# Kernel tuning notes

Measured on AMD Instinct MI355X. Metric: run time of the kernel, lower is better.

The kernel has to match this reference:

```python
import jax, jax.numpy as jnp
import numpy as np

N = 50000
E = 800000
D_IN, D_HID, D_OUT = 128, 128, 64
BN_EPS = 1e-5

def _glorot(key, shape):
    fan_in = shape[-1]
    return jax.random.normal(key, shape, dtype=jnp.float32) / jnp.sqrt(jnp.float32(fan_in))

def setup_inputs() -> dict:
    key = jax.random.key(0)
    ks = jax.random.split(key, 16)
    x = jax.random.normal(ks[0], (N, D_IN), dtype=jnp.float32)
    edge_index = jax.random.randint(ks[1], (2, E), 0, N, dtype=jnp.int64)
    edge_pairs = jax.random.randint(ks[2], (2, E), 0, N, dtype=jnp.int64)
    return {
        "x": x,
        "edge_index": edge_index,
        "edge_pairs": edge_pairs,
        # SAGEConv1: lin_l (bias) on aggregated neighbors, lin_r (no bias) on root
        "c1_Wl": _glorot(ks[3], (D_HID, D_IN)),
        "c1_bl": jnp.zeros((D_HID,), jnp.float32),
        "c1_Wr": _glorot(ks[4], (D_HID, D_IN)),
        # BatchNorm1d (eval mode: running stats)
        "bn_gamma": jnp.ones((D_HID,), jnp.float32),
        "bn_beta": jnp.zeros((D_HID,), jnp.float32),
        "bn_mean": jnp.zeros((D_HID,), jnp.float32),
        "bn_var": jnp.ones((D_HID,), jnp.float32),
        # SAGEConv2
        "c2_Wl": _glorot(ks[5], (D_OUT, D_HID)),
        "c2_bl": jnp.zeros((D_OUT,), jnp.float32),
        "c2_Wr": _glorot(ks[6], (D_OUT, D_HID)),
        # EdgeRegHead MLP: Linear(2*D_OUT, D_OUT) -> ReLU -> Linear(D_OUT, D_OUT//2) -> ReLU -> Linear(D_OUT//2, 1) -> Sigmoid
        "e_W1": _glorot(ks[7], (D_OUT, 2 * D_OUT)),
        "e_b1": jnp.zeros((D_OUT,), jnp.float32),
        "e_W2": _glorot(ks[8], (D_OUT // 2, D_OUT)),
        "e_b2": jnp.zeros((D_OUT // 2,), jnp.float32),
        "e_W3": _glorot(ks[9], (1, D_OUT // 2)),
        "e_b3": jnp.zeros((1,), jnp.float32),
    }

def _sage_conv(x, src, dst, Wl, bl, Wr):
    # mean-aggregate source features at destination nodes (PyG SAGEConv mean aggr)
    msg_sum = jax.ops.segment_sum(x[src], dst, num_segments=N)          # [N, d]
    cnt = jax.ops.segment_sum(jnp.ones((src.shape[0],), x.dtype), dst, num_segments=N)
    mean = msg_sum / jnp.maximum(cnt, 1.0)[:, None]
    return mean @ Wl.T + bl + x @ Wr.T

def reference(x, edge_index, edge_pairs,
              c1_Wl, c1_bl, c1_Wr,
              bn_gamma, bn_beta, bn_mean, bn_var,
              c2_Wl, c2_bl, c2_Wr,
              e_W1, e_b1, e_W2, e_b2, e_W3, e_b3):
    src, dst = edge_index[0], edge_index[1]
    h = _sage_conv(x, src, dst, c1_Wl, c1_bl, c1_Wr)                    # [N, D_HID]
    h = (h - bn_mean) * jax.lax.rsqrt(bn_var + BN_EPS) * bn_gamma + bn_beta
    h = jax.nn.relu(h)                                                   # dropout inactive (eval)
    z = _sage_conv(h, src, dst, c2_Wl, c2_bl, c2_Wr)                    # [N, D_OUT]
    zi = z[edge_pairs[0]]                                               # [P, D_OUT]
    zj = z[edge_pairs[1]]
    e = jnp.concatenate([zi, zj], axis=-1)                              # [P, 2*D_OUT]
    e = jax.nn.relu(e @ e_W1.T + e_b1)
    e = jax.nn.relu(e @ e_W2.T + e_b2)
    return jax.nn.sigmoid(e @ e_W3.T + e_b3)                            # [P, 1]
```

## Files before the change

### kernel.cpp

```cpp
#include <hip/hip_runtime.h>
#include <hip/hip_bf16.h>
#include <math.h>

#define NN 50000
#define NE 800000
#define DIN 128
#define DHID 128
#define DOUT 64
#define BN_EPS 1e-5f

typedef __attribute__((ext_vector_type(8))) short bf16x8;
typedef __attribute__((ext_vector_type(8))) _Float16 f16x8;
typedef __attribute__((ext_vector_type(4))) _Float16 f16x4;
typedef __attribute__((ext_vector_type(2))) _Float16 f16x2;
typedef __attribute__((ext_vector_type(4))) float f32x4;
typedef unsigned short ushort_t;
typedef unsigned int uint_t;

__device__ __forceinline__ ushort_t f2bf(float f) {
    uint_t u = __float_as_uint(f);
    uint_t r = (u + 0x7FFFu + ((u >> 16) & 1u)) >> 16;
    return (ushort_t)r;
}

__device__ __forceinline__ uint_t pk2bf(float a, float b) {
    __hip_bfloat16 x = __float2bfloat16(a);
    __hip_bfloat16 y = __float2bfloat16(b);
    ushort_t ux = *reinterpret_cast<ushort_t*>(&x);
    ushort_t uy = *reinterpret_cast<ushort_t*>(&y);
    return (uint_t)ux | ((uint_t)uy << 16);
}

__global__ __launch_bounds__(256) void k_deg_xcast(
    const int* __restrict__ ei, int* __restrict__ deg,
    const float* __restrict__ x, _Float16* __restrict__ xh)
{
    int b = blockIdx.x;
    if (b < 3125) {
        int e = b * 256 + threadIdx.x;
        atomicAdd(deg + ei[NE + e], 1);
    } else {
        int i = (b - 3125) * 256 + threadIdx.x;
        const float4* src = (const float4*)x + (size_t)i * 2;
        float4 a = src[0], c = src[1];
        f16x8 o;
        o[0] = (_Float16)a.x; o[1] = (_Float16)a.y; o[2] = (_Float16)a.z; o[3] = (_Float16)a.w;
        o[4] = (_Float16)c.x; o[5] = (_Float16)c.y; o[6] = (_Float16)c.z; o[7] = (_Float16)c.w;
        *(f16x8*)(xh + (size_t)i * 8) = o;
    }
}

__global__ __launch_bounds__(256) void k_scan1_prep(
    const int* __restrict__ deg, int* __restrict__ part,
    const float* __restrict__ c1_Wl, const float* __restrict__ c1_Wr,
    const float* __restrict__ c2_Wl, const float* __restrict__ c2_Wr,
    const float* __restrict__ gam, const float* __restrict__ bet,
    const float* __restrict__ bmean, const float* __restrict__ bvar,
    const float* __restrict__ eW1, const float* __restrict__ eW2,
    _Float16* __restrict__ w1cat, _Float16* __restrict__ w2cat,
    ushort_t* __restrict__ w1bf, ushort_t* __restrict__ w2bf,
    float* __restrict__ bnsc, float* __restrict__ bnsh)
{
    int t = threadIdx.x;
    if (blockIdx.x < 49) {
        __shared__ int s[256];
        int g = blockIdx.x * 256 + t;
        int v = 0;
        if (g < 12500) { int4 d = ((const int4*)deg)[g]; v = d.x + d.y + d.z + d.w; }
        s[t] = v;
        __syncthreads();
        #pragma unroll
        for (int off = 128; off > 0; off >>= 1) {
            if (t < off) s[t] += s[t + off];
            __syncthreads();
        }
        if (t == 0) part[blockIdx.x] = s[0];
    } else {
        for (int i = t; i < 128 * 128; i += 256) {
            int row = i >> 7, k = i & 127;
            w1cat[row * 256 + k]       = (_Float16)c1_Wl[i];
            w1cat[row * 256 + 128 + k] = (_Float16)c1_Wr[i];
        }
        for (int i = t; i < 64 * 128; i += 256) {
            int row = i >> 7, k = i & 127;
            w2cat[row * 256 + k]       = (_Float16)c2_Wl[i];
            w2cat[row * 256 + 128 + k] = (_Float16)c2_Wr[i];
        }
        for (int i = t; i < 64 * 128; i += 256) w1bf[i] = f2bf(eW1[i]);
        for (int i = t; i < 32 * 64; i += 256)  w2bf[i] = f2bf(eW2[i]);
        for (int i = t; i < 128; i += 256) {
            float s = gam[i] * rsqrtf(bvar[i] + BN_EPS);
            bnsc[i] = s;
            bnsh[i] = bet[i] - bmean[i] * s;
        }
    }
}

__global__ __launch_bounds__(256) void k_scan3(
    const int* __restrict__ deg, const int* __restrict__ part, int* __restrict__ rowptr)
{
    __shared__ int s[256];
    __shared__ int p[64];
    int t = threadIdx.x;
    int b = blockIdx.x;
    int g = b * 256 + t;
    int4 d = make_int4(0, 0, 0, 0);
    if (g < 12500) d = ((const int4*)deg)[g];
    int sum4 = d.x + d.y + d.z + d.w;
    s[t] = sum4;
    if (t < 49) p[t] = part[t];
    __syncthreads();
    #pragma unroll
    for (int off = 1; off < 256; off <<= 1) {
        int v = (t >= off) ? s[t - off] : 0;
        __syncthreads();
        s[t] += v;
        __syncthreads();
    }
    int blockoff = 0;
    for (int i = 0; i < b; ++i) blockoff += p[i];
    int off0 = blockoff + s[t] - sum4;
    if (g < 12500) {
        int4 o;
        o.x = off0;
        o.y = off0 + d.x;
        o.z = o.y + d.y;
        o.w = o.z + d.z;
        ((int4*)rowptr)[g] = o;
        if (g == 12499) rowptr[NN] = o.w + d.w;
    }
}

__global__ __launch_bounds__(256) void k_fill(
    const int* __restrict__ ei, const int* __restrict__ rowptr,
    int* __restrict__ cursor, int* __restrict__ csr_src)
{
    int e = blockIdx.x * blockDim.x + threadIdx.x;
    if (e >= NE) return;
    int dst = ei[NE + e];
    int slot = atomicAdd(cursor + dst, 1);
    csr_src[rowptr[dst] + slot] = ei[e];
}

#define GATHER4_128(feat)                                                      \
    {                                                                          \
        _Pragma("unroll 1")                                                    \
        for (int q = 0; q < 4; ++q) {                                          \
            int n = w * 4 + q;                                                 \
            int node4 = tile * 16 + n;                                         \
            int beg = __builtin_amdgcn_readfirstlane(rowptr[node4]);           \
            int end = __builtin_amdgcn_readfirstlane(rowptr[node4 + 1]);       \
            float2 a0 = {0.f,0.f}, a1 = {0.f,0.f}, a2 = {0.f,0.f}, a3 = {0.f,0.f}; \
            float2 a4 = {0.f,0.f}, a5 = {0.f,0.f}, a6 = {0.f,0.f}, a7 = {0.f,0.f}; \
            int j = beg;                                                       \
            for (; j + 7 < end; j += 8) {                                      \
                int s0 = csr_src[j];     int s1 = csr_src[j + 1];              \
                int s2 = csr_src[j + 2]; int s3 = csr_src[j + 3];              \
                int s4 = csr_src[j + 4]; int s5 = csr_src[j + 5];              \
                int s6 = csr_src[j + 6]; int s7 = csr_src[j + 7];              \
                f16x2 v0 = *(const f16x2*)(feat + (size_t)s0 * 128 + lane * 2);\
                f16x2 v1 = *(const f16x2*)(feat + (size_t)s1 * 128 + lane * 2);\
                f16x2 v2 = *(const f16x2*)(feat + (size_t)s2 * 128 + lane * 2);\
                f16x2 v3 = *(const f16x2*)(feat + (size_t)s3 * 128 + lane * 2);\
                f16x2 v4 = *(const f16x2*)(feat + (size_t)s4 * 128 + lane * 2);\
                f16x2 v5 = *(const f16x2*)(feat + (size_t)s5 * 128 + lane * 2);\
                f16x2 v6 = *(const f16x2*)(feat + (size_t)s6 * 128 + lane * 2);\
                f16x2 v7 = *(const f16x2*)(feat + (size_t)s7 * 128 + lane * 2);\
                a0.x += (float)v0[0]; a0.y += (float)v0[1];                    \
                a1.x += (float)v1[0]; a1.y += (float)v1[1];                    \
                a2.x += (float)v2[0]; a2.y += (float)v2[1];                    \
                a3.x += (float)v3[0]; a3.y += (float)v3[1];                    \
                a4.x += (float)v4[0]; a4.y += (float)v4[1];                    \
                a5.x += (float)v5[0]; a5.y += (float)v5[1];                    \
                a6.x += (float)v6[0]; a6.y += (float)v6[1];                    \
                a7.x += (float)v7[0]; a7.y += (float)v7[1];                    \
            }                                                                  \
            for (; j + 1 < end; j += 2) {                                      \
                int s0 = csr_src[j];                                           \
                int s1 = csr_src[j + 1];                                       \
                f16x2 v0 = *(const f16x2*)(feat + (size_t)s0 * 128 + lane * 2);\
                f16x2 v1 = *(const f16x2*)(feat + (size_t)s1 * 128 + lane * 2);\
                a0.x += (float)v0[0]; a0.y += (float)v0[1];                    \
                a1.x += (float)v1[0]; a1.y += (float)v1[1];                    \
            }                                                                  \
            if (j < end) {                                                     \
                int s0 = csr_src[j];                                           \
                f16x2 v0 = *(const f16x2*)(feat + (size_t)s0 * 128 + lane * 2);\
                a0.x += (float)v0[0]; a0.y += (float)v0[1];                    \
            }                                                                  \
            float inv = 1.0f / fmaxf((float)(end - beg), 1.0f);                \
            f16x2 o;                                                           \
            o[0] = (_Float16)((a0.x + a1.x + a2.x + a3.x + a4.x + a5.x + a6.x + a7.x) * inv); \
            o[1] = (_Float16)((a0.y + a1.y + a2.y + a3.y + a4.y + a5.y + a6.y + a7.y) * inv); \
            uint_t off = (uint_t)(n * 256 + lane * 4) ^ (uint_t)((n & 7) << 4);\
            *(f16x2*)((char*)mlds + off) = o;                                  \
        }                                                                      \
    }

__global__ __launch_bounds__(256) void k_gconv1(
    const _Float16* __restrict__ xh, const int* __restrict__ rowptr,
    const int* __restrict__ csr_src,
    const _Float16* __restrict__ w1cat, const float* __restrict__ bl,
    const float* __restrict__ bnsc, const float* __restrict__ bnsh,
    _Float16* __restrict__ hh)
{
    __shared__ _Float16 mlds[16 * 128];
    const int tid = threadIdx.x;
    const int lane = tid & 63;
    const int w = tid >> 6;
    const int tile = blockIdx.x;
    const int e = lane & 15;
    const int c = lane >> 4;
    const int node = tile * 16 + e;

    f16x8 wf[2][8];
    #pragma unroll
    for (int nt = 0; nt < 2; ++nt)
        #pragma unroll
        for (int ks = 0; ks < 8; ++ks)
            wf[nt][ks] = *(const f16x8*)(w1cat + (size_t)(w * 32 + nt * 16 + e) * 256 + ks * 32 + c * 8);
    f16x8 bfx[4];
    #pragma unroll
    for (int ks = 0; ks < 4; ++ks)
        bfx[ks] = *(const f16x8*)(xh + (size_t)node * 128 + ks * 32 + c * 8);
    f32x4 acc[2];
    #pragma unroll
    for (int nt = 0; nt < 2; ++nt)
        acc[nt] = *(const f32x4*)(bl + w * 32 + nt * 16 + c * 4);

    GATHER4_128(xh);
    __syncthreads();

    f16x8 bfm[4];
    #pragma unroll
    for (int ks = 0; ks < 4; ++ks) {
        uint_t off = (uint_t)(e * 256 + ks * 64 + c * 16) ^ (uint_t)((e & 7) << 4);
        bfm[ks] = *(const f16x8*)((const char*)mlds + off);
    }

    #pragma unroll
    for (int ks = 0; ks < 4; ++ks)
        #pragma unroll
        for (int nt = 0; nt < 2; ++nt)
            acc[nt] = __builtin_amdgcn_mfma_f32_16x16x32_f16(wf[nt][ks], bfm[ks], acc[nt], 0, 0, 0);
    #pragma unroll
    for (int ks = 0; ks < 4; ++ks)
        #pragma unroll
        for (int nt = 0; nt < 2; ++nt)
            acc[nt] = __builtin_amdgcn_mfma_f32_16x16x32_f16(wf[nt][ks + 4], bfx[ks], acc[nt], 0, 0, 0);

    #pragma unroll
    for (int nt = 0; nt < 2; ++nt) {
        int j0 = w * 32 + nt * 16 + c * 4;
        f32x4 sc = *(const f32x4*)(bnsc + j0);
        f32x4 sh = *(const f32x4*)(bnsh + j0);
        f16x4 o;
        #pragma unroll
        for (int r = 0; r < 4; ++r)
            o[r] = (_Float16)fmaxf(acc[nt][r] * sc[r] + sh[r], 0.f);
        *(f16x4*)(hh + (size_t)node * 128 + j0) = o;
    }
}

__global__ __launch_bounds__(256) void k_hw(
    const _Float16* __restrict__ hh, const _Float16* __restrict__ w2cat,
    _Float16* __restrict__ hw)
{
    const int tid = threadIdx.x;
    const int lane = tid & 63;
    const int e = lane & 15;
    const int c = lane >> 4;
    const int w = tid >> 6;
    const int node = blockIdx.x * 16 + e;

    f16x8 wf[4];
    #pragma unroll
    for (int ks = 0; ks < 4; ++ks)
        wf[ks] = *(const f16x8*)(w2cat + (size_t)(w * 16 + e) * 256 + ks * 32 + c * 8);
    f16x8 bf[4];
    #pragma unroll
    for (int ks = 0; ks < 4; ++ks)
        bf[ks] = *(const f16x8*)(hh + (size_t)node * 128 + ks * 32 + c * 8);

    f32x4 acc = {0.f, 0.f, 0.f, 0.f};
    #pragma unroll
    for (int ks = 0; ks < 4; ++ks)
        acc = __builtin_amdgcn_mfma_f32_16x16x32_f16(wf[ks], bf[ks], acc, 0, 0, 0);

    f16x4 o;
    #pragma unroll
    for (int r = 0; r < 4; ++r) o[r] = (_Float16)acc[r];
    *(f16x4*)(hw + (size_t)node * 64 + w * 16 + c * 4) = o;
}

__global__ __launch_bounds__(256) void k_gconv2(
    const _Float16* __restrict__ hh, const _Float16* __restrict__ hw,
    const int* __restrict__ rowptr, const int* __restrict__ csr_src,
    const _Float16* __restrict__ w2cat, const float* __restrict__ bl,
    ushort_t* __restrict__ zbf)
{
    __shared__ float mlds32[16 * 64];
    const int tid = threadIdx.x;
    const int lane = tid & 63;
    const int w = tid >> 6;
    const int tile = blockIdx.x;
    const int e = lane & 15;
    const int c = lane >> 4;
    const int node = tile * 16 + e;

    f16x8 wf[4];
    #pragma unroll
    for (int ks = 0; ks < 4; ++ks)
        wf[ks] = *(const f16x8*)(w2cat + (size_t)(w * 16 + e) * 256 + 128 + ks * 32 + c * 8);
    f16x8 bfx[4];
    #pragma unroll
    for (int ks = 0; ks < 4; ++ks)
        bfx[ks] = *(const f16x8*)(hh + (size_t)node * 128 + ks * 32 + c * 8);

    #pragma unroll 1
    for (int q = 0; q < 4; ++q) {
        int n = w * 4 + q;
        int node4 = tile * 16 + n;
        int beg = __builtin_amdgcn_readfirstlane(rowptr[node4]);
        int end = __builtin_amdgcn_readfirstlane(rowptr[node4 + 1]);
        float a0 = 0.f, a1 = 0.f, a2 = 0.f, a3 = 0.f;
        float a4 = 0.f, a5 = 0.f, a6 = 0.f, a7 = 0.f;
        int j = beg;
        for (; j + 7 < end; j += 8) {
            int s0 = csr_src[j];     int s1 = csr_src[j + 1];
            int s2 = csr_src[j + 2]; int s3 = csr_src[j + 3];
            int s4 = csr_src[j + 4]; int s5 = csr_src[j + 5];
            int s6 = csr_src[j + 6]; int s7 = csr_src[j + 7];
            a0 += (float)hw[(size_t)s0 * 64 + lane];
            a1 += (float)hw[(size_t)s1 * 64 + lane];
            a2 += (float)hw[(size_t)s2 * 64 + lane];
            a3 += (float)hw[(size_t)s3 * 64 + lane];
            a4 += (float)hw[(size_t)s4 * 64 + lane];
            a5 += (float)hw[(size_t)s5 * 64 + lane];
            a6 += (float)hw[(size_t)s6 * 64 + lane];
            a7 += (float)hw[(size_t)s7 * 64 + lane];
        }
        for (; j + 1 < end; j += 2) {
            int s0 = csr_src[j];
            int s1 = csr_src[j + 1];
            a0 += (float)hw[(size_t)s0 * 64 + lane];
            a1 += (float)hw[(size_t)s1 * 64 + lane];
        }
        if (j < end) {
            int s0 = csr_src[j];
            a0 += (float)hw[(size_t)s0 * 64 + lane];
        }
        float inv = 1.0f / fmaxf((float)(end - beg), 1.0f);
        float m = (a0 + a1 + a2 + a3 + a4 + a5 + a6 + a7) * inv;
        uint_t off = (uint_t)(n * 256 + lane * 4) ^ (uint_t)((n & 7) << 4);
        *(float*)((char*)mlds32 + off) = m;
    }
    __syncthreads();

    f32x4 acc = *(const f32x4*)(bl + w * 16 + c * 4);
    {
        uint_t off = (uint_t)(e * 256 + (w * 16 + c * 4) * 4) ^ (uint_t)((e & 7) << 4);
        f32x4 mv = *(const f32x4*)((const char*)mlds32 + off);
        acc[0] += mv[0]; acc[1] += mv[1]; acc[2] += mv[2]; acc[3] += mv[3];
    }

    #pragma unroll
    for (int ks = 0; ks < 4; ++ks)
        acc = __builtin_amdgcn_mfma_f32_16x16x32_f16(wf[ks], bfx[ks], acc, 0, 0, 0);

    int j0 = w * 16 + c * 4;
    uint2 pk;
    pk.x = pk2bf(acc[0], acc[1]);
    pk.y = pk2bf(acc[2], acc[3]);
    *(uint2*)(zbf + (size_t)node * 64 + j0) = pk;
}

__global__ __launch_bounds__(256) void k_edge(
    const ushort_t* __restrict__ zbf, const int* __restrict__ ep,
    const ushort_t* __restrict__ w1bf, const float* __restrict__ b1,
    const ushort_t* __restrict__ w2bf, const float* __restrict__ b2,
    const float* __restrict__ W3, const float* __restrict__ b3,
    float* __restrict__ out)
{
    __shared__ ushort_t a1lds[4][16 * 64];
    const int tid  = threadIdx.x;
    const int lane = tid & 63;
    const int e    = lane & 15;
    const int c    = lane >> 4;
    ushort_t* lds  = &a1lds[tid >> 6][0];
    const uint_t swz = (uint_t)((e & 7) << 4);

    bf16x8 w1f[4][4];
    #pragma unroll
    for (int mt = 0; mt < 4; ++mt)
        #pragma unroll
        for (int ks = 0; ks < 4; ++ks)
            w1f[mt][ks] = *(const bf16x8*)(w1bf + (mt * 16 + e) * 128 + ks * 32 + c * 8);

    bf16x8 w2f[2][2];
    #pragma unroll
    for (int mt2 = 0; mt2 < 2; ++mt2)
        #pragma unroll
        for (int ks2 = 0; ks2 < 2; ++ks2)
            w2f[mt2][ks2] = *(const bf16x8*)(w2bf + (mt2 * 16 + e) * 64 + ks2 * 32 + c * 8);

    f32x4 bias1[4];
    #pragma unroll
    for (int mt = 0; mt < 4; ++mt) bias1[mt] = *(const f32x4*)(b1 + mt * 16 + c * 4);
    f32x4 bias2[2];
    #pragma unroll
    for (int mt2 = 0; mt2 < 2; ++mt2) bias2[mt2] = *(const f32x4*)(b2 + mt2 * 16 + c * 4);
    f32x4 w3v[2];
    #pragma unroll
    for (int mt2 = 0; mt2 < 2; ++mt2) w3v[mt2] = *(const f32x4*)(W3 + mt2 * 16 + c * 4);
    const float b3v = b3[0];

    const int nw = (gridDim.x * blockDim.x) >> 6;
    const int NT = NE / 16;

#define LOADZ(T, dst)                                                         \
    {                                                                         \
        int p = (T) * 16 + e;                                                 \
        int ni = ep[p];                                                       \
        int nj = ep[NE + p];                                                  \
        const ushort_t* zi = zbf + (size_t)ni * DOUT;                         \
        const ushort_t* zj = zbf + (size_t)nj * DOUT;                         \
        dst[0] = *(const bf16x8*)(zi + c * 8);                                \
        dst[1] = *(const bf16x8*)(zi + 32 + c * 8);                           \
        dst[2] = *(const bf16x8*)(zj + c * 8);                                \
        dst[3] = *(const bf16x8*)(zj + 32 + c * 8);                           \
    }

#define COMPUTE(T, bfr)                                                       \
    {                                                                         \
        f32x4 acc[4];                                                         \
        _Pragma("unroll")                                                     \
        for (int mt = 0; mt < 4; ++mt) acc[mt] = bias1[mt];                   \
        _Pragma("unroll")                                                     \
        for (int ks = 0; ks < 4; ++ks)                                        \
            _Pragma("unroll")                                                 \
            for (int mt = 0; mt < 4; ++mt)                                    \
                acc[mt] = __builtin_amdgcn_mfma_f32_16x16x32_bf16(            \
                    w1f[mt][ks], bfr[ks], acc[mt], 0, 0, 0);                  \
        _Pragma("unroll")                                                     \
        for (int mt = 0; mt < 4; ++mt) {                                      \
            uint_t lo = pk2bf(fmaxf(acc[mt][0], 0.f), fmaxf(acc[mt][1], 0.f));\
            uint_t hi = pk2bf(fmaxf(acc[mt][2], 0.f), fmaxf(acc[mt][3], 0.f));\
            uint_t off = (uint_t)(e * 128 + mt * 32 + c * 8) ^ swz;           \
            *(uint2*)((char*)lds + off) = make_uint2(lo, hi);                 \
        }                                                                     \
        bf16x8 b2f[2];                                                        \
        _Pragma("unroll")                                                     \
        for (int ks2 = 0; ks2 < 2; ++ks2) {                                   \
            uint_t off = (uint_t)(e * 128 + ks2 * 64 + c * 16) ^ swz;         \
            b2f[ks2] = *(const bf16x8*)((const char*)lds + off);              \
        }                                                                     \
        f32x4 a2[2];                                                          \
        _Pragma("unroll")                                                     \
        for (int mt2 = 0; mt2 < 2; ++mt2) a2[mt2] = bias2[mt2];               \
        _Pragma("unroll")                                                     \
        for (int ks2 = 0; ks2 < 2; ++ks2)                                     \
            _Pragma("unroll")                                                 \
            for (int mt2 = 0; mt2 < 2; ++mt2)                                 \
                a2[mt2] = __builtin_amdgcn_mfma_f32_16x16x32_bf16(            \
                    w2f[mt2][ks2], b2f[ks2], a2[mt2], 0, 0, 0);               \
        float t3 = b3v;                                                       \
        _Pragma("unroll")                                                     \
        for (int mt2 = 0; mt2 < 2; ++mt2)                                     \
            _Pragma("unroll")                                                 \
            for (int r = 0; r < 4; ++r)                                       \
                t3 += fmaxf(a2[mt2][r], 0.f) * w3v[mt2][r];                   \
        t3 += __shfl_xor(t3, 16);                                             \
        t3 += __shfl_xor(t3, 32);                                             \
        if (lane < 16) {                                                      \
            float ex = __expf(-t3);                                           \
            out[(T) * 16 + lane] = __builtin_amdgcn_rcpf(1.f + ex);           \
        }                                                                     \
    }

    bf16x8 zA[4], zB[4];
    int tile = (blockIdx.x * blockDim.x + tid) >> 6;
    if (tile >= NT) return;
    LOADZ(tile, zA);
    while (tile < NT) {
        int nx = tile + nw;
        if (nx < NT) LOADZ(nx, zB);
        COMPUTE(tile, zA);
        tile = nx;
        if (tile >= NT) break;
        nx = tile + nw;
        if (nx < NT) LOADZ(nx, zA);
        COMPUTE(tile, zB);
        tile = nx;
    }

#undef LOADZ
#undef COMPUTE
}

extern "C" void kernel_launch(void* const* d_in, const int* in_sizes, int n_in,
                              void* d_out, int out_size, void* d_ws, size_t ws_size,
                              hipStream_t stream)
{
    const float* x     = (const float*)d_in[0];
    const int*   ei    = (const int*)d_in[1];
    const int*   ep    = (const int*)d_in[2];
    const float* c1_Wl = (const float*)d_in[3];
    const float* c1_bl = (const float*)d_in[4];
    const float* c1_Wr = (const float*)d_in[5];
    const float* bn_g  = (const float*)d_in[6];
    const float* bn_b  = (const float*)d_in[7];
    const float* bn_m  = (const float*)d_in[8];
    const float* bn_v  = (const float*)d_in[9];
    const float* c2_Wl = (const float*)d_in[10];
    const float* c2_bl = (const float*)d_in[11];
    const float* c2_Wr = (const float*)d_in[12];
    const float* e_W1  = (const float*)d_in[13];
    const float* e_b1  = (const float*)d_in[14];
    const float* e_W2  = (const float*)d_in[15];
    const float* e_b2  = (const float*)d_in[16];
    const float* e_W3  = (const float*)d_in[17];
    const float* e_b3  = (const float*)d_in[18];
    float* out = (float*)d_out;

    _Float16* xh    = (_Float16*)d_ws;
    _Float16* hwbuf = xh + (size_t)NN * DIN;
    _Float16* hh    = hwbuf + (size_t)NN * DIN;
    ushort_t* zbf   = (ushort_t*)(hh + (size_t)NN * DHID);
    _Float16* w1cat = (_Float16*)(zbf + (size_t)NN * DOUT);
    _Float16* w2cat = w1cat + 128 * 256;
    ushort_t* w1bf  = (ushort_t*)(w2cat + 64 * 256);
    ushort_t* w2bf  = w1bf + 64 * 128;
    float*    bnsc  = (float*)(w2bf + 32 * 64);
    float*    bnsh  = bnsc + 128;
    int*      deg     = (int*)(bnsh + 128);
    int*      cursor  = deg + 50048;
    int*      rowptr  = cursor + 50048;
    int*      csr_src = rowptr + 50052;
    int*      part    = csr_src + 800000;

    hipMemsetAsync(deg, 0, (size_t)(50048 * 2) * sizeof(int), stream);

    k_deg_xcast<<<6250, 256, 0, stream>>>(ei, deg, x, xh);
    k_scan1_prep<<<50, 256, 0, stream>>>(deg, part,
                                         c1_Wl, c1_Wr, c2_Wl, c2_Wr,
                                         bn_g, bn_b, bn_m, bn_v, e_W1, e_W2,
                                         w1cat, w2cat, w1bf, w2bf, bnsc, bnsh);
    k_scan3<<<49, 256, 0, stream>>>(deg, part, rowptr);
    k_fill <<<3125, 256, 0, stream>>>(ei, rowptr, cursor, csr_src);

    k_gconv1<<<3125, 256, 0, stream>>>(xh, rowptr, csr_src, w1cat, c1_bl, bnsc, bnsh, hh);
    k_hw    <<<3125, 256, 0, stream>>>(hh, w2cat, hwbuf);
    k_gconv2<<<3125, 256, 0, stream>>>(hh, hwbuf, rowptr, csr_src, w2cat, c2_bl, zbf);

    k_edge<<<1024, 256, 0, stream>>>(zbf, ep, w1bf, e_b1, w2bf, e_b2,
                                     e_W3, e_b3, out);
}
```

Baseline: 284.0 us.

## Fuse hidden-to-output projection into gconv1 and triple-buffer edge head loads

The separate k_hw kernel is folded into k_gconv1. Each block now writes its 16x128 post-BN/ReLU hidden tile into a swizzled LDS buffer and immediately multiplies it by the second-layer weights, so the hidden tile is not re-read from global memory and one launch goes away. The edge MLP kernel moves from double- to triple-buffered z-row gathers so more loads are in flight while computing. The trade-off is extra LDS, a block barrier and more registers in gconv1, plus more registers in k_edge, which may reduce occupancy.

```diff
diff --git a/kernel.cpp b/kernel.cpp
--- a/kernel.cpp
+++ b/kernel.cpp
@@ -202,9 +202,11 @@
     const int* __restrict__ csr_src,
     const _Float16* __restrict__ w1cat, const float* __restrict__ bl,
     const float* __restrict__ bnsc, const float* __restrict__ bnsh,
-    _Float16* __restrict__ hh)
+    const _Float16* __restrict__ w2cat, _Float16* __restrict__ hh,
+    _Float16* __restrict__ hw)
 {
     __shared__ _Float16 mlds[16 * 128];
+    __shared__ _Float16 hlds[16 * 128];
     const int tid = threadIdx.x;
     const int lane = tid & 63;
     const int w = tid >> 6;
@@ -259,38 +261,31 @@
         for (int r = 0; r < 4; ++r)
             o[r] = (_Float16)fmaxf(acc[nt][r] * sc[r] + sh[r], 0.f);
         *(f16x4*)(hh + (size_t)node * 128 + j0) = o;
-    }
-}
-
-__global__ __launch_bounds__(256) void k_hw(
-    const _Float16* __restrict__ hh, const _Float16* __restrict__ w2cat,
-    _Float16* __restrict__ hw)
-{
-    const int tid = threadIdx.x;
-    const int lane = tid & 63;
-    const int e = lane & 15;
-    const int c = lane >> 4;
-    const int w = tid >> 6;
-    const int node = blockIdx.x * 16 + e;
-
-    f16x8 wf[4];
-    #pragma unroll
-    for (int ks = 0; ks < 4; ++ks)
-        wf[ks] = *(const f16x8*)(w2cat + (size_t)(w * 16 + e) * 256 + ks * 32 + c * 8);
-    f16x8 bf[4];
-    #pragma unroll
-    for (int ks = 0; ks < 4; ++ks)
-        bf[ks] = *(const f16x8*)(hh + (size_t)node * 128 + ks * 32 + c * 8);
-
-    f32x4 acc = {0.f, 0.f, 0.f, 0.f};
-    #pragma unroll
-    for (int ks = 0; ks < 4; ++ks)
-        acc = __builtin_amdgcn_mfma_f32_16x16x32_f16(wf[ks], bf[ks], acc, 0, 0, 0);
-
-    f16x4 o;
-    #pragma unroll
-    for (int r = 0; r < 4; ++r) o[r] = (_Float16)acc[r];
-    *(f16x4*)(hw + (size_t)node * 64 + w * 16 + c * 4) = o;
+        uint_t hoff = (uint_t)(e * 256 + j0 * 2) ^ (uint_t)((e & 7) << 4);
+        *(f16x4*)((char*)hlds + hoff) = o;
+    }
+
+    f16x8 wf2[4];
+    #pragma unroll
+    for (int ks = 0; ks < 4; ++ks)
+        wf2[ks] = *(const f16x8*)(w2cat + (size_t)(w * 16 + e) * 256 + ks * 32 + c * 8);
+    __syncthreads();
+
+    f16x8 bfh[4];
+    #pragma unroll
+    for (int ks = 0; ks < 4; ++ks) {
+        uint_t off = (uint_t)(e * 256 + ks * 64 + c * 16) ^ (uint_t)((e & 7) << 4);
+        bfh[ks] = *(const f16x8*)((const char*)hlds + off);
+    }
+    f32x4 acc2 = {0.f, 0.f, 0.f, 0.f};
+    #pragma unroll
+    for (int ks = 0; ks < 4; ++ks)
+        acc2 = __builtin_amdgcn_mfma_f32_16x16x32_f16(wf2[ks], bfh[ks], acc2, 0, 0, 0);
+
+    f16x4 ohw;
+    #pragma unroll
+    for (int r = 0; r < 4; ++r) ohw[r] = (_Float16)acc2[r];
+    *(f16x4*)(hw + (size_t)node * 64 + w * 16 + c * 4) = ohw;
 }
 
 __global__ __launch_bounds__(256) void k_gconv2(
@@ -478,20 +473,27 @@
         }                                                                     \
     }
 
-    bf16x8 zA[4], zB[4];
-    int tile = (blockIdx.x * blockDim.x + tid) >> 6;
-    if (tile >= NT) return;
-    LOADZ(tile, zA);
-    while (tile < NT) {
-        int nx = tile + nw;
-        if (nx < NT) LOADZ(nx, zB);
-        COMPUTE(tile, zA);
-        tile = nx;
-        if (tile >= NT) break;
-        nx = tile + nw;
-        if (nx < NT) LOADZ(nx, zA);
-        COMPUTE(tile, zB);
-        tile = nx;
+    bf16x8 zA[4], zB[4], zC[4];
+    int ta = (blockIdx.x * blockDim.x + tid) >> 6;
+    if (ta >= NT) return;
+    int tb = ta + nw;
+    int tc = tb + nw;
+    LOADZ(ta, zA);
+    if (tb < NT) LOADZ(tb, zB);
+    if (tc < NT) LOADZ(tc, zC);
+    while (true) {
+        COMPUTE(ta, zA);
+        ta += 3 * nw;
+        if (ta < NT) LOADZ(ta, zA);
+        if (tb >= NT) break;
+        COMPUTE(tb, zB);
+        tb += 3 * nw;
+        if (tb < NT) LOADZ(tb, zB);
+        if (tc >= NT) break;
+        COMPUTE(tc, zC);
+        tc += 3 * nw;
+        if (tc < NT) LOADZ(tc, zC);
+        if (ta >= NT) break;
     }
 
 #undef LOADZ
@@ -549,8 +551,8 @@
     k_scan3<<<49, 256, 0, stream>>>(deg, part, rowptr);
     k_fill <<<3125, 256, 0, stream>>>(ei, rowptr, cursor, csr_src);
 
-    k_gconv1<<<3125, 256, 0, stream>>>(xh, rowptr, csr_src, w1cat, c1_bl, bnsc, bnsh, hh);
-    k_hw    <<<3125, 256, 0, stream>>>(hh, w2cat, hwbuf);
+    k_gconv1<<<3125, 256, 0, stream>>>(xh, rowptr, csr_src, w1cat, c1_bl,
+                                       bnsc, bnsh, w2cat, hh, hwbuf);
     k_gconv2<<<3125, 256, 0, stream>>>(hh, hwbuf, rowptr, csr_src, w2cat, c2_bl, zbf);
 
     k_edge<<<1024, 256, 0, stream>>>(zbf, ep, w1bf, e_b1, w2bf, e_b2,
```

After: 280.6 us. About the same (-1.2%).
